# Optimization experiments

Measured on AMD Instinct MI355X. Metric: run time of the kernel, lower is better.

Reference implementation:

```python
import jax, jax.numpy as jnp
import numpy as np

NUM_USERS = 100000
NUM_ITEMS = 50000
N = NUM_USERS + NUM_ITEMS
D = 64
L = 3
E = 2400000


def setup_inputs() -> dict:
    key = jax.random.key(0)
    ks = jax.random.split(key, 5)
    edge_index = jax.random.randint(ks[0], (2, E), 0, N, dtype=jnp.int32)
    user_emb = jax.random.normal(ks[1], (NUM_USERS, D), dtype=jnp.float32) * 0.1
    item_emb = jax.random.normal(ks[2], (NUM_ITEMS, D), dtype=jnp.float32) * 0.1
    Ws = jax.random.normal(ks[3], (L, D, D), dtype=jnp.float32) * (1.0 / np.sqrt(D))
    bs = jax.random.normal(ks[4], (L, D), dtype=jnp.float32) * 0.01
    return {"edge_index": edge_index, "user_emb": user_emb, "item_emb": item_emb,
            "Ws": Ws, "bs": bs}


def _gcn_conv(x, W, b, src, dst):
    # PyG GCNConv: h = x @ W; add self-loops; sym-normalize; aggregate at dst; + bias
    h = x @ W                                      # [N, D]
    loop = jnp.arange(N, dtype=src.dtype)
    s = jnp.concatenate([src, loop])               # [E+N]
    d = jnp.concatenate([dst, loop])
    ones = jnp.ones(s.shape[0], dtype=x.dtype)
    deg = jax.ops.segment_sum(ones, d, num_segments=N)          # in-degree incl. self-loop
    dinv = jnp.where(deg > 0, jax.lax.rsqrt(deg), 0.0)
    norm = dinv[s] * dinv[d]                       # [E+N]
    msg = h[s] * norm[:, None]                     # gather + scale  [E+N, D]
    out = jax.ops.segment_sum(msg, d, num_segments=N)            # scatter-add at dst
    return out + b


def reference(edge_index, user_emb, item_emb, Ws, bs):
    src, dst = edge_index[0], edge_index[1]
    x = jnp.concatenate([user_emb, item_emb], axis=0)  # [N, D]
    acc = x
    for l in range(L):
        x = _gcn_conv(x, Ws[l], bs[l], src, dst)
        acc = acc + x
    emb = acc / (L + 1)                              # mean over layer outputs
    return emb[:NUM_USERS], emb[NUM_USERS:]
```

## Files before the change

### kernel.cpp

```cpp
#include <hip/hip_runtime.h>

constexpr int D = 64;
constexpr int BUK_SHIFT = 9;
constexpr int BUK_NODES = 1 << BUK_SHIFT;
constexpr int MAX_NBUK = 320;
constexpr int CAP = 10240;
constexpr int TILE_E = 4096;

typedef __attribute__((ext_vector_type(8))) short short8;
typedef __attribute__((ext_vector_type(4))) float f32x4;

__device__ inline unsigned short f2bf(float f) {
    unsigned int u = __float_as_uint(f);
    u += 0x7FFFu + ((u >> 16) & 1u);
    return (unsigned short)(u >> 16);
}
__device__ inline float bf2f(unsigned short s) {
    return __uint_as_float(((unsigned int)s) << 16);
}
__device__ inline float ub0(unsigned int q) { return (float)(q & 0xffu); }
__device__ inline float ub1(unsigned int q) { return (float)((q >> 8) & 0xffu); }
__device__ inline float ub2(unsigned int q) { return (float)((q >> 16) & 0xffu); }
__device__ inline float ub3(unsigned int q) { return (float)(q >> 24); }

__global__ __launch_bounds__(512) void k_scatter_direct(const int* __restrict__ ei,
                                                        int* __restrict__ gfill,
                                                        unsigned int* __restrict__ packed,
                                                        int E, int nbuk) {
    __shared__ int hist[MAX_NBUK];
    const int tid = threadIdx.x;
    for (int i = tid; i < nbuk; i += 512) hist[i] = 0;
    __syncthreads();

    const int t0 = blockIdx.x * TILE_E;
    int bk[8];
    unsigned int vv[8];
#pragma unroll
    for (int j = 0; j < 8; ++j) {
        int e = t0 + tid + j * 512;
        bk[j] = -1;
        if (e < E) {
            int src = ei[e];
            int dst = ei[E + e];
            bk[j] = dst >> BUK_SHIFT;
            vv[j] = ((unsigned int)(dst & (BUK_NODES - 1)) << 18) | (unsigned int)src;
            atomicAdd(&hist[bk[j]], 1);
        }
    }
    __syncthreads();
    for (int i = tid; i < nbuk; i += 512) {
        int h = hist[i];
        hist[i] = h ? atomicAdd(&gfill[i], h) : 0;
    }
    __syncthreads();
#pragma unroll
    for (int j = 0; j < 8; ++j) {
        if (bk[j] >= 0) {
            int b = bk[j];
            int pos = atomicAdd(&hist[b], 1);
            if (pos < CAP) packed[(size_t)b * CAP + pos] = vv[j];
        }
    }
}

__global__ __launch_bounds__(256) void k_build_csr(const unsigned int* __restrict__ packed,
                                                   const int* __restrict__ gfill,
                                                   unsigned int* __restrict__ rowpk,
                                                   float* __restrict__ dinv,
                                                   int* __restrict__ csr_src,
                                                   int N) {
    __shared__ int hist[BUK_NODES], rp[BUK_NODES];
    const int b = blockIdx.x;
    const int s = b * CAP;
    const int cnt = min(gfill[b], CAP);
    const int tid = threadIdx.x;
    for (int i = tid; i < BUK_NODES; i += 256) hist[i] = 0;
    __syncthreads();
    for (int e = tid; e < cnt; e += 256)
        atomicAdd(&hist[packed[s + e] >> 18], 1);
    __syncthreads();
    if (tid == 0) {
        int run = 0;
        for (int i = 0; i < BUK_NODES; ++i) { rp[i] = run; run += hist[i]; }
    }
    __syncthreads();
    const int dbase = b << BUK_SHIFT;
    for (int ld = tid; ld < BUK_NODES; ld += 256) {
        int d = dbase + ld;
        if (d < N) {
            rowpk[d] = ((unsigned int)(s + rp[ld]) << 10) | (unsigned int)hist[ld];
            dinv[d] = rsqrtf((float)(hist[ld] + 1));
        }
    }
    __syncthreads();
    for (int e = tid; e < cnt; e += 256) {
        unsigned int v = packed[s + e];
        int ld = v >> 18;
        int pos = s + atomicAdd(&rp[ld], 1);
        csr_src[pos] = (int)(v & 0x3FFFFu);
    }
}

template <bool F32IN>
__global__ __launch_bounds__(256) void k_gemm(const float* __restrict__ u,
                                              const float* __restrict__ it,
                                              int U,
                                              const unsigned short* __restrict__ xin16,
                                              const float* __restrict__ W,
                                              const float* __restrict__ dinv,
                                              unsigned char* __restrict__ X8,
                                              float* __restrict__ S,
                                              int N) {
    const int lane = threadIdx.x & 63;
    const int g = lane >> 4;
    const int lr = lane & 15;

    short8 bf[4][2];
#pragma unroll
    for (int ct = 0; ct < 4; ++ct)
#pragma unroll
        for (int kb = 0; kb < 2; ++kb) {
            short8 v;
            int c = ct * 16 + lr;
#pragma unroll
            for (int e = 0; e < 4; ++e) {
                int k0 = kb * 32 + g * 4 + e;
                v[e]     = (short)f2bf(W[k0 * D + c]);
                v[e + 4] = (short)f2bf(W[(k0 + 16) * D + c]);
            }
            bf[ct][kb] = v;
        }

    const int wid = blockIdx.x * (blockDim.x >> 6) + (threadIdx.x >> 6);
    const int nw = gridDim.x * (blockDim.x >> 6);

    for (int rb = wid * 16; rb < N; rb += nw * 16) {
        int row = rb + lr;
        bool ok = (row < N);
        short8 af[2];
        if (F32IN) {
            const float* xr = nullptr;
            if (ok) xr = (row < U) ? (u + (size_t)row * D)
                                   : (it + (size_t)(row - U) * D);
#pragma unroll
            for (int kb = 0; kb < 2; ++kb) {
                float4 q0 = ok ? *(const float4*)(xr + kb * 32 + g * 4)
                               : float4{0.f, 0.f, 0.f, 0.f};
                float4 q1 = ok ? *(const float4*)(xr + kb * 32 + 16 + g * 4)
                               : float4{0.f, 0.f, 0.f, 0.f};
                short8 v;
                v[0] = (short)f2bf(q0.x); v[1] = (short)f2bf(q0.y);
                v[2] = (short)f2bf(q0.z); v[3] = (short)f2bf(q0.w);
                v[4] = (short)f2bf(q1.x); v[5] = (short)f2bf(q1.y);
                v[6] = (short)f2bf(q1.z); v[7] = (short)f2bf(q1.w);
                af[kb] = v;
            }
        } else {
            const unsigned short* xr = xin16 + (size_t)row * D;
#pragma unroll
            for (int kb = 0; kb < 2; ++kb) {
                short4 q0 = ok ? *(const short4*)(xr + kb * 32 + g * 4)
                               : short4{0, 0, 0, 0};
                short4 q1 = ok ? *(const short4*)(xr + kb * 32 + 16 + g * 4)
                               : short4{0, 0, 0, 0};
                short8 v;
                v[0] = q0.x; v[1] = q0.y; v[2] = q0.z; v[3] = q0.w;
                v[4] = q1.x; v[5] = q1.y; v[6] = q1.z; v[7] = q1.w;
                af[kb] = v;
            }
        }

        float di[4];
#pragma unroll
        for (int r = 0; r < 4; ++r) {
            int ro = rb + g * 4 + r;
            di[r] = (ro < N) ? dinv[ro] : 0.f;
        }

        float vals[4][4];
        float mx = 0.f;
#pragma unroll
        for (int ct = 0; ct < 4; ++ct) {
            f32x4 a = {0.f, 0.f, 0.f, 0.f};
            a = __builtin_amdgcn_mfma_f32_16x16x32_bf16(af[0], bf[ct][0], a, 0, 0, 0);
            a = __builtin_amdgcn_mfma_f32_16x16x32_bf16(af[1], bf[ct][1], a, 0, 0, 0);
#pragma unroll
            for (int r = 0; r < 4; ++r) {
                float v = a[r] * di[r];
                vals[ct][r] = v;
                mx = fmaxf(mx, fabsf(v));
            }
        }
#pragma unroll
        for (int off = 32; off > 0; off >>= 1)
            mx = fmaxf(mx, __shfl_xor(mx, off));
        mx = fmaxf(mx, 1e-30f);
        const float sinv = 127.0f / mx;
        if (lane == 0) S[rb >> 4] = mx * (1.0f / 127.0f);
#pragma unroll
        for (int ct = 0; ct < 4; ++ct)
#pragma unroll
            for (int r = 0; r < 4; ++r) {
                int ro = rb + g * 4 + r;
                if (ro < N)
                    X8[(size_t)ro * D + ct * 16 + lr] =
                        (unsigned char)(int)(rintf(vals[ct][r] * sinv) + 128.f);
            }
    }
}

template <bool LAST>
__global__ __launch_bounds__(256) void k_aggregate(const unsigned int* __restrict__ rowpk,
                                                   const int* __restrict__ csr_src,
                                                   const unsigned char* __restrict__ X8,
                                                   const float* __restrict__ S,
                                                   const float* __restrict__ dinv,
                                                   const float* __restrict__ b,
                                                   unsigned short* __restrict__ val16,
                                                   const float* __restrict__ u,
                                                   const float* __restrict__ it,
                                                   int U,
                                                   const unsigned short* __restrict__ V1,
                                                   const unsigned short* __restrict__ V2,
                                                   float* __restrict__ acc,
                                                   int N) {
    int w = (int)((blockIdx.x * (size_t)blockDim.x + threadIdx.x) >> 6);
    int lane = threadIdx.x & 63;
    if (w >= N) return;
    const int es = lane >> 4;
    const int lc = lane & 15;
    const unsigned int* Q = (const unsigned int*)X8;
    unsigned int pk = rowpk[w];
    int beg = (int)(pk >> 10);
    int end = beg + (int)(pk & 1023u);
    const float di = dinv[w];

    float a0 = 0.f, a1 = 0.f, a2 = 0.f, a3 = 0.f, as = 0.f;
    if (es == 0) {
        unsigned int q = Q[(size_t)w * 16 + lc];
        float s = S[w >> 4];
        a0 = fmaf(ub0(q), s, a0); a1 = fmaf(ub1(q), s, a1);
        a2 = fmaf(ub2(q), s, a2); a3 = fmaf(ub3(q), s, a3);
        as += s;
    }

    int e = beg;
    for (; e + 16 <= end; e += 16) {
        int idx[4];
#pragma unroll
        for (int j = 0; j < 4; ++j) idx[j] = csr_src[e + 4 * j + es];
        unsigned int q[4];
#pragma unroll
        for (int j = 0; j < 4; ++j) q[j] = Q[(size_t)idx[j] * 16 + lc];
        float s[4];
#pragma unroll
        for (int j = 0; j < 4; ++j) s[j] = S[idx[j] >> 4];
#pragma unroll
        for (int j = 0; j < 4; ++j) {
            a0 = fmaf(ub0(q[j]), s[j], a0);
            a1 = fmaf(ub1(q[j]), s[j], a1);
            a2 = fmaf(ub2(q[j]), s[j], a2);
            a3 = fmaf(ub3(q[j]), s[j], a3);
            as += s[j];
        }
    }
    for (; e + 4 <= end; e += 4) {
        int idx = csr_src[e + es];
        unsigned int q = Q[(size_t)idx * 16 + lc];
        float s = S[idx >> 4];
        a0 = fmaf(ub0(q), s, a0); a1 = fmaf(ub1(q), s, a1);
        a2 = fmaf(ub2(q), s, a2); a3 = fmaf(ub3(q), s, a3);
        as += s;
    }
    int rem = end - e;
    if (es < rem) {
        int idx = csr_src[e + es];
        unsigned int q = Q[(size_t)idx * 16 + lc];
        float s = S[idx >> 4];
        a0 = fmaf(ub0(q), s, a0); a1 = fmaf(ub1(q), s, a1);
        a2 = fmaf(ub2(q), s, a2); a3 = fmaf(ub3(q), s, a3);
        as += s;
    }

    const float bias128 = 128.f * as;
    a0 -= bias128; a1 -= bias128; a2 -= bias128; a3 -= bias128;
#pragma unroll
    for (int off = 16; off <= 32; off <<= 1) {
        a0 += __shfl_xor(a0, off);
        a1 += __shfl_xor(a1, off);
        a2 += __shfl_xor(a2, off);
        a3 += __shfl_xor(a3, off);
    }

    if (es == 0) {
        float4 bb = *(const float4*)(b + 4 * lc);
        float v0 = fmaf(a0, di, bb.x);
        float v1 = fmaf(a1, di, bb.y);
        float v2 = fmaf(a2, di, bb.z);
        float v3 = fmaf(a3, di, bb.w);
        if (LAST) {
            const float* x0 = (w < U) ? (u + (size_t)w * D)
                                      : (it + (size_t)(w - U) * D);
            float4 x = *(const float4*)(x0 + 4 * lc);
            ushort4 p1 = *(const ushort4*)(V1 + (size_t)w * D + 4 * lc);
            ushort4 p2 = *(const ushort4*)(V2 + (size_t)w * D + 4 * lc);
            float4 o;
            o.x = (x.x + bf2f(p1.x) + bf2f(p2.x) + v0) * 0.25f;
            o.y = (x.y + bf2f(p1.y) + bf2f(p2.y) + v1) * 0.25f;
            o.z = (x.z + bf2f(p1.z) + bf2f(p2.z) + v2) * 0.25f;
            o.w = (x.w + bf2f(p1.w) + bf2f(p2.w) + v3) * 0.25f;
            *(float4*)(acc + (size_t)w * D + 4 * lc) = o;
        } else {
            ushort4 pk4;
            pk4.x = f2bf(v0); pk4.y = f2bf(v1); pk4.z = f2bf(v2); pk4.w = f2bf(v3);
            *(ushort4*)(val16 + (size_t)w * D + 4 * lc) = pk4;
        }
    }
}

extern "C" void kernel_launch(void* const* d_in, const int* in_sizes, int n_in,
                              void* d_out, int out_size, void* d_ws, size_t ws_size,
                              hipStream_t stream) {
    const int* ei      = (const int*)d_in[0];
    const float* uemb  = (const float*)d_in[1];
    const float* iemb  = (const float*)d_in[2];
    const float* Ws    = (const float*)d_in[3];
    const float* bs    = (const float*)d_in[4];

    const int E = in_sizes[0] / 2;
    const int U = in_sizes[1] / D;
    const int I = in_sizes[2] / D;
    const int N = U + I;
    const int ND = N * D;
    const int nbuk = (N + BUK_NODES - 1) >> BUK_SHIFT;
    const int NT = (N + 15) / 16;

    unsigned char* X8 = (unsigned char*)d_ws;
    float* S = (float*)(X8 + ND);
    unsigned short* V1 = (unsigned short*)(S + ((NT + 1) & ~1));
    unsigned short* V2 = V1 + ND;
    float* dinv    = (float*)(V2 + ND);
    int*   csr_src = (int*)(dinv + N);
    unsigned int* packed = (unsigned int*)(csr_src + (size_t)nbuk * CAP);
    unsigned int* rowpk  = packed + (size_t)nbuk * CAP;
    int*   gfill   = (int*)(rowpk + N);

    float* acc = (float*)d_out;

    hipMemsetAsync(gfill, 0, nbuk * sizeof(int), stream);
    k_scatter_direct<<<(E + TILE_E - 1) / TILE_E, 512, 0, stream>>>(ei, gfill, packed,
                                                                    E, nbuk);
    k_build_csr<<<nbuk, 256, 0, stream>>>(packed, gfill, rowpk, dinv, csr_src, N);

    const int nagg = (N + 3) / 4;
    k_gemm<true><<<1024, 256, 0, stream>>>(uemb, iemb, U, nullptr, Ws, dinv, X8, S, N);
    k_aggregate<false><<<nagg, 256, 0, stream>>>(rowpk, csr_src, X8, S, dinv, bs, V1,
                                                 nullptr, nullptr, U, nullptr, nullptr,
                                                 nullptr, N);
    k_gemm<false><<<1024, 256, 0, stream>>>(nullptr, nullptr, U, V1,
                                            Ws + (size_t)1 * D * D, dinv, X8, S, N);
    k_aggregate<false><<<nagg, 256, 0, stream>>>(rowpk, csr_src, X8, S, dinv, bs + D, V2,
                                                 nullptr, nullptr, U, nullptr, nullptr,
                                                 nullptr, N);
    k_gemm<false><<<1024, 256, 0, stream>>>(nullptr, nullptr, U, V2,
                                            Ws + (size_t)2 * D * D, dinv, X8, S, N);
    k_aggregate<true><<<nagg, 256, 0, stream>>>(rowpk, csr_src, X8, S, dinv, bs + 2 * D,
                                                nullptr, uemb, iemb, U, V1, V2, acc, N);
}
```

Before: 319.3 us.

## Stage scatter edges in LDS sorted by bucket and parallelize CSR prefix scan

The scatter kernel now keeps per-edge local ranks, runs an exclusive scan over bucket counts, sorts the tile's edges by bucket in shared memory, and then writes them to global memory in contiguous runs instead of issuing a per-edge shared atomic followed by a scattered store. The CSR build kernel replaces a single-thread serial prefix sum over 512 node counts with a parallel Hillis-Steele scan across 256 threads. The aim is more coalesced global writes and less serial work, at the cost of more LDS use (about 26KB), which may lower occupancy, and extra barriers.

```diff
diff --git a/kernel.cpp b/kernel.cpp
--- a/kernel.cpp
+++ b/kernel.cpp
@@ -28,12 +28,16 @@
                                                         unsigned int* __restrict__ packed,
                                                         int E, int nbuk) {
     __shared__ int hist[MAX_NBUK];
+    __shared__ int gbase[MAX_NBUK];
+    __shared__ int sc[512];
+    __shared__ unsigned int sm_e[TILE_E];
+    __shared__ unsigned short sm_b[TILE_E];
     const int tid = threadIdx.x;
     for (int i = tid; i < nbuk; i += 512) hist[i] = 0;
     __syncthreads();
 
     const int t0 = blockIdx.x * TILE_E;
-    int bk[8];
+    int bk[8], rk[8];
     unsigned int vv[8];
 #pragma unroll
     for (int j = 0; j < 8; ++j) {
@@ -44,22 +48,41 @@
             int dst = ei[E + e];
             bk[j] = dst >> BUK_SHIFT;
             vv[j] = ((unsigned int)(dst & (BUK_NODES - 1)) << 18) | (unsigned int)src;
-            atomicAdd(&hist[bk[j]], 1);
-        }
-    }
-    __syncthreads();
-    for (int i = tid; i < nbuk; i += 512) {
-        int h = hist[i];
-        hist[i] = h ? atomicAdd(&gfill[i], h) : 0;
-    }
-    __syncthreads();
+            rk[j] = atomicAdd(&hist[bk[j]], 1);
+        }
+    }
+    __syncthreads();
+
+    int c = (tid < nbuk) ? hist[tid] : 0;
+    sc[tid] = c;
+    __syncthreads();
+    for (int off = 1; off < 512; off <<= 1) {
+        int t = (tid >= off) ? sc[tid - off] : 0;
+        __syncthreads();
+        sc[tid] += t;
+        __syncthreads();
+    }
+    if (tid < nbuk) {
+        hist[tid] = sc[tid] - c;
+        gbase[tid] = c ? atomicAdd(&gfill[tid], c) : 0;
+    }
+    __syncthreads();
+    const int cnt = sc[511];
+
 #pragma unroll
     for (int j = 0; j < 8; ++j) {
         if (bk[j] >= 0) {
-            int b = bk[j];
-            int pos = atomicAdd(&hist[b], 1);
-            if (pos < CAP) packed[(size_t)b * CAP + pos] = vv[j];
-        }
+            int pos = hist[bk[j]] + rk[j];
+            sm_e[pos] = vv[j];
+            sm_b[pos] = (unsigned short)bk[j];
+        }
+    }
+    __syncthreads();
+
+    for (int i = tid; i < cnt; i += 512) {
+        int b = sm_b[i];
+        int gpos = gbase[b] + (i - hist[b]);
+        if (gpos < CAP) packed[(size_t)b * CAP + gpos] = sm_e[i];
     }
 }
 
@@ -69,7 +92,7 @@
                                                    float* __restrict__ dinv,
                                                    int* __restrict__ csr_src,
                                                    int N) {
-    __shared__ int hist[BUK_NODES], rp[BUK_NODES];
+    __shared__ int hist[BUK_NODES], rp[BUK_NODES], part[256];
     const int b = blockIdx.x;
     const int s = b * CAP;
     const int cnt = min(gfill[b], CAP);
@@ -79,11 +102,21 @@
     for (int e = tid; e < cnt; e += 256)
         atomicAdd(&hist[packed[s + e] >> 18], 1);
     __syncthreads();
-    if (tid == 0) {
-        int run = 0;
-        for (int i = 0; i < BUK_NODES; ++i) { rp[i] = run; run += hist[i]; }
-    }
-    __syncthreads();
+
+    int h0 = hist[tid * 2], h1 = hist[tid * 2 + 1];
+    part[tid] = h0 + h1;
+    __syncthreads();
+    for (int off = 1; off < 256; off <<= 1) {
+        int t = (tid >= off) ? part[tid - off] : 0;
+        __syncthreads();
+        part[tid] += t;
+        __syncthreads();
+    }
+    int run = part[tid] - (h0 + h1);
+    rp[tid * 2] = run;
+    rp[tid * 2 + 1] = run + h0;
+    __syncthreads();
+
     const int dbase = b << BUK_SHIFT;
     for (int ld = tid; ld < BUK_NODES; ld += 256) {
         int d = dbase + ld;
```

After: 309.9 us. 2.9% less time.
